# Kernel optimization log

Hardware: AMD Instinct MI355X
Metric: run time of the kernel (lower is better)

Reference implementation:

```python
import jax, jax.numpy as jnp
import numpy as np

B, S, D = 4, 512, 128


def setup_inputs() -> dict:
    key = jax.random.key(0)
    ks = jax.random.split(key, 9)
    scale = 1.0 / np.sqrt(D)
    return {
        "inputs": jax.random.normal(ks[0], (B, S, D), dtype=jnp.float32),
        "encoder_outputs": jax.random.normal(ks[1], (B, S, D), dtype=jnp.float32),
        "mask": jax.random.randint(ks[2], (B, S), 0, 2, dtype=jnp.int32),
        "W1": jax.random.uniform(ks[3], (D, D), jnp.float32, -scale, scale),
        "b1": jax.random.uniform(ks[4], (D,), jnp.float32, -scale, scale),
        "W2": jax.random.uniform(ks[5], (D, D), jnp.float32, -scale, scale),
        "b2": jax.random.uniform(ks[6], (D,), jnp.float32, -scale, scale),
        "v_w": jax.random.uniform(ks[7], (D,), jnp.float32, -scale, scale),
        "v_b": jax.random.uniform(ks[8], (1,), jnp.float32, -scale, scale),
    }


def reference(inputs, encoder_outputs, mask, W1, b1, W2, b2, v_w, v_b):
    # key_out: W1(encoder_outputs)  [B, S_k, D]
    key_out = jnp.einsum("bkd,de->bke", encoder_outputs, W1) + b1
    # query_out: W2(inputs)        [B, S_q, D]
    query_out = jnp.einsum("bqd,de->bqe", inputs, W2) + b2
    # additive attention, all query positions at once: [B, S_q, S_k, D]
    t = jnp.tanh(key_out[:, None, :, :] + query_out[:, :, None, :])
    ui = jnp.einsum("bqkd,d->bqk", t, v_w) + v_b[0]
    # mask out padded key positions for every query position
    valid = mask.astype(bool)[:, None, :]  # [B, 1, S_k]
    logits = jnp.where(valid, ui, -jnp.inf)
    preds = jnp.argmax(logits, axis=-1)
    return (logits, preds)
```

## Files before the change

### kernel.cpp

```cpp
#include <hip/hip_runtime.h>
#include <math.h>

#define NB 4
#define NS 512
#define ND 128
#define ND4 32

static constexpr float K2LE = 2.885390081777927f;

__device__ inline float fast_exp2(float x){
#if __has_builtin(__builtin_amdgcn_exp2f)
  return __builtin_amdgcn_exp2f(x);
#else
  float r; asm("v_exp_f32 %0, %1" : "=v"(r) : "v"(x)); return r;
#endif
}
__device__ inline float fast_rcp(float x){
#if __has_builtin(__builtin_amdgcn_rcpf)
  return __builtin_amdgcn_rcpf(x);
#else
  float r; asm("v_rcp_f32 %0, %1" : "=v"(r) : "v"(x)); return r;
#endif
}

__global__ __launch_bounds__(256) void proj_kernel(
    const float* __restrict__ inputs, const float* __restrict__ enc,
    const float* __restrict__ W1, const float* __restrict__ b1,
    const float* __restrict__ W2, const float* __restrict__ b2,
    const float* __restrict__ vw, const float* __restrict__ vb,
    float* __restrict__ EKT4, float* __restrict__ RQ, float* __restrict__ WQ,
    float* __restrict__ Csum){
  int blk = blockIdx.x;
  int t = threadIdx.x;

  if (blk == 512){
    if (t < 64){
      float v = vw[t] + vw[t + 64];
      #pragma unroll
      for (int off = 32; off; off >>= 1) v += __shfl_down(v, off);
      if (t == 0) Csum[0] = v + vb[0];
    }
    return;
  }

  bool is_key = (blk < 256);
  int rbase = (is_key ? blk : blk - 256) * 8;
  const float* X    = is_key ? enc : inputs;
  const float* W    = is_key ? W1  : W2;
  const float* bias = is_key ? b1  : b2;

  __shared__ float rows[8][132];
  {
    int r = t >> 5, c4 = (t & 31) * 4;
    *(float4*)&rows[r][c4] = *(const float4*)(X + (size_t)(rbase + r)*ND + c4);
  }
  __syncthreads();

  int rg = t >> 5;
  int ec = (t & 31) * 4;
  float4 acc = *(const float4*)(bias + ec);
  #pragma unroll 2
  for (int d4 = 0; d4 < ND4; ++d4){
    float4 x4 = *(const float4*)&rows[rg][4*d4];
    const float* wp = W + (size_t)(4*d4)*ND + ec;
    float4 w0 = *(const float4*)(wp);
    float4 w1 = *(const float4*)(wp + ND);
    float4 w2 = *(const float4*)(wp + 2*ND);
    float4 w3 = *(const float4*)(wp + 3*ND);
    acc.x = fmaf(x4.x, w0.x, acc.x); acc.y = fmaf(x4.x, w0.y, acc.y);
    acc.z = fmaf(x4.x, w0.z, acc.z); acc.w = fmaf(x4.x, w0.w, acc.w);
    acc.x = fmaf(x4.y, w1.x, acc.x); acc.y = fmaf(x4.y, w1.y, acc.y);
    acc.z = fmaf(x4.y, w1.z, acc.z); acc.w = fmaf(x4.y, w1.w, acc.w);
    acc.x = fmaf(x4.z, w2.x, acc.x); acc.y = fmaf(x4.z, w2.y, acc.y);
    acc.z = fmaf(x4.z, w2.z, acc.z); acc.w = fmaf(x4.z, w2.w, acc.w);
    acc.x = fmaf(x4.w, w3.x, acc.x); acc.y = fmaf(x4.w, w3.y, acc.y);
    acc.z = fmaf(x4.w, w3.z, acc.z); acc.w = fmaf(x4.w, w3.w, acc.w);
  }

  if (is_key){
    int b    = rbase >> 9;
    int sloc = rbase & (NS - 1);
    __syncthreads();
    rows[rg][ec+0] = fast_exp2(K2LE*acc.x);
    rows[rg][ec+1] = fast_exp2(K2LE*acc.y);
    rows[rg][ec+2] = fast_exp2(K2LE*acc.z);
    rows[rg][ec+3] = fast_exp2(K2LE*acc.w);
    __syncthreads();
    int d4 = t >> 3, sl = t & 7;
    float4 v = *(const float4*)&rows[sl][4*d4];
    ((float4*)EKT4)[((size_t)(b*ND4 + d4))*NS + sloc + sl] = v;
  } else {
    int row = rbase + rg;
    float4 vw4 = *(const float4*)(vw + ec);
    float4 r4, w4;
    r4.x = fast_exp2(-K2LE*acc.x);
    r4.y = fast_exp2(-K2LE*acc.y);
    r4.z = fast_exp2(-K2LE*acc.z);
    r4.w = fast_exp2(-K2LE*acc.w);
    w4.x = -2.0f*vw4.x*r4.x;
    w4.y = -2.0f*vw4.y*r4.y;
    w4.z = -2.0f*vw4.z*r4.z;
    w4.w = -2.0f*vw4.w*r4.w;
    *(float4*)(RQ + (size_t)row*ND + ec) = r4;
    *(float4*)(WQ + (size_t)row*ND + ec) = w4;
  }
}

__global__ __launch_bounds__(512) void score_kernel(
    const float* __restrict__ EKT4, const float* __restrict__ RQg,
    const float* __restrict__ WQg, const int* __restrict__ mask,
    const float* __restrict__ Csum, float* __restrict__ out){
  int blk = blockIdx.x;
  int b  = blk >> 7;
  int q0 = (blk & 127) * 4;
  int t  = threadIdx.x;

  const float4* ek4 = (const float4*)EKT4 + (size_t)(b*ND4)*NS + t;
  const float* rq = RQg + (size_t)(b*NS + q0)*ND;
  const float* wq = WQg + (size_t)(b*NS + q0)*ND;

  float C = Csum[0];
  int m = mask[b*NS + t];

  float a0=0.f, a1=0.f, a2=0.f, a3=0.f;
  #pragma unroll 2
  for (int d4 = 0; d4 < ND4; ++d4){
    float4 ek = ek4[(size_t)d4*NS];
    int d = 4*d4;
    float4 r0 = *(const float4*)(rq + d);
    float4 r1 = *(const float4*)(rq + ND + d);
    float4 r2 = *(const float4*)(rq + 2*ND + d);
    float4 r3 = *(const float4*)(rq + 3*ND + d);
    float4 w0 = *(const float4*)(wq + d);
    float4 w1 = *(const float4*)(wq + ND + d);
    float4 w2 = *(const float4*)(wq + 2*ND + d);
    float4 w3 = *(const float4*)(wq + 3*ND + d);
    a0 = fmaf(w0.x, fast_rcp(ek.x + r0.x), a0);
    a0 = fmaf(w0.y, fast_rcp(ek.y + r0.y), a0);
    a0 = fmaf(w0.z, fast_rcp(ek.z + r0.z), a0);
    a0 = fmaf(w0.w, fast_rcp(ek.w + r0.w), a0);
    a1 = fmaf(w1.x, fast_rcp(ek.x + r1.x), a1);
    a1 = fmaf(w1.y, fast_rcp(ek.y + r1.y), a1);
    a1 = fmaf(w1.z, fast_rcp(ek.z + r1.z), a1);
    a1 = fmaf(w1.w, fast_rcp(ek.w + r1.w), a1);
    a2 = fmaf(w2.x, fast_rcp(ek.x + r2.x), a2);
    a2 = fmaf(w2.y, fast_rcp(ek.y + r2.y), a2);
    a2 = fmaf(w2.z, fast_rcp(ek.z + r2.z), a2);
    a2 = fmaf(w2.w, fast_rcp(ek.w + r2.w), a2);
    a3 = fmaf(w3.x, fast_rcp(ek.x + r3.x), a3);
    a3 = fmaf(w3.y, fast_rcp(ek.y + r3.y), a3);
    a3 = fmaf(w3.z, fast_rcp(ek.z + r3.z), a3);
    a3 = fmaf(w3.w, fast_rcp(ek.w + r3.w), a3);
  }

  const float NINF = -3.0e38f;
  float u[4];
  u[0] = m ? (C + a0) : NINF;
  u[1] = m ? (C + a1) : NINF;
  u[2] = m ? (C + a2) : NINF;
  u[3] = m ? (C + a3) : NINF;

  float* logits = out;
  float* preds  = out + (size_t)NB*NS*NS;
  {
    size_t base = (size_t)(b*NS + q0) * NS + t;
    logits[base]        = u[0];
    logits[base +   NS] = u[1];
    logits[base + 2*NS] = u[2];
    logits[base + 3*NS] = u[3];
  }

  int lane = t & 63, wv = t >> 6;
  __shared__ float red_v[8][4];
  __shared__ int   red_i[8][4];
  #pragma unroll
  for (int qi = 0; qi < 4; ++qi){
    float v = u[qi]; int idx = t;
    #pragma unroll
    for (int off = 32; off; off >>= 1){
      float ov = __shfl_down(v, off);
      int   oi = __shfl_down(idx, off);
      if (ov > v || (ov == v && oi < idx)){ v = ov; idx = oi; }
    }
    if (lane == 0){ red_v[wv][qi] = v; red_i[wv][qi] = idx; }
  }
  __syncthreads();
  if (t < 4){
    float v = red_v[0][t]; int idx = red_i[0][t];
    #pragma unroll
    for (int w = 1; w < 8; ++w){
      float ov = red_v[w][t]; int oi = red_i[w][t];
      if (ov > v || (ov == v && oi < idx)){ v = ov; idx = oi; }
    }
    preds[b*NS + q0 + t] = (float)idx;
  }
}

extern "C" void kernel_launch(void* const* d_in, const int* in_sizes, int n_in,
                              void* d_out, int out_size, void* d_ws, size_t ws_size,
                              hipStream_t stream){
  const float* inputs = (const float*)d_in[0];
  const float* enc    = (const float*)d_in[1];
  const int*   mask   = (const int*)d_in[2];
  const float* W1     = (const float*)d_in[3];
  const float* b1     = (const float*)d_in[4];
  const float* W2     = (const float*)d_in[5];
  const float* b2     = (const float*)d_in[6];
  const float* vw     = (const float*)d_in[7];
  const float* vb     = (const float*)d_in[8];
  float* out = (float*)d_out;

  float* ws   = (float*)d_ws;
  float* EKT4 = ws;
  float* RQ   = ws + 262144;
  float* WQ   = ws + 524288;
  float* Cs   = ws + 786432;

  proj_kernel <<<dim3(513), dim3(256), 0, stream>>>(inputs, enc, W1, b1, W2, b2,
                                                    vw, vb, EKT4, RQ, WQ, Cs);
  score_kernel<<<dim3(512), dim3(512), 0, stream>>>(EKT4, RQ, WQ, mask, Cs, out);
}
```

Before: 99.72 us.

## Split score kernel over key tiles with atomic argmax merge

```diff
diff --git a/kernel.cpp b/kernel.cpp
--- a/kernel.cpp
+++ b/kernel.cpp
@@ -5,6 +5,8 @@
 #define NS 512
 #define ND 128
 #define ND4 32
+#define KT 256
+#define NKT (NS/KT)
 
 static constexpr float K2LE = 2.885390081777927f;
 
@@ -23,17 +25,24 @@
 #endif
 }
 
+__device__ inline unsigned enc_f32(float f){
+  unsigned u = __float_as_uint(f);
+  return (u & 0x80000000u) ? ~u : (u | 0x80000000u);
+}
+
 __global__ __launch_bounds__(256) void proj_kernel(
     const float* __restrict__ inputs, const float* __restrict__ enc,
     const float* __restrict__ W1, const float* __restrict__ b1,
     const float* __restrict__ W2, const float* __restrict__ b2,
     const float* __restrict__ vw, const float* __restrict__ vb,
     float* __restrict__ EKT4, float* __restrict__ RQ, float* __restrict__ WQ,
-    float* __restrict__ Csum){
+    float* __restrict__ Csum, unsigned long long* __restrict__ Amax){
   int blk = blockIdx.x;
   int t = threadIdx.x;
 
   if (blk == 512){
+    #pragma unroll
+    for (int i = t; i < NB*NS; i += 256) Amax[i] = 0ull;
     if (t < 64){
       float v = vw[t] + vw[t + 64];
       #pragma unroll
@@ -106,21 +115,25 @@
   }
 }
 
-__global__ __launch_bounds__(512) void score_kernel(
+__global__ __launch_bounds__(256) void score_kernel(
     const float* __restrict__ EKT4, const float* __restrict__ RQg,
     const float* __restrict__ WQg, const int* __restrict__ mask,
-    const float* __restrict__ Csum, float* __restrict__ out){
+    const float* __restrict__ Csum, float* __restrict__ out,
+    unsigned long long* __restrict__ Amax){
   int blk = blockIdx.x;
-  int b  = blk >> 7;
-  int q0 = (blk & 127) * 4;
-  int t  = threadIdx.x;
-
-  const float4* ek4 = (const float4*)EKT4 + (size_t)(b*ND4)*NS + t;
+  int b   = blk >> 8;
+  int rem = blk & 255;
+  int q0  = (rem >> 1) * 4;
+  int kt  = rem & 1;
+  int t   = threadIdx.x;
+  int k   = kt*KT + t;
+
+  const float4* ek4 = (const float4*)EKT4 + (size_t)(b*ND4)*NS + k;
   const float* rq = RQg + (size_t)(b*NS + q0)*ND;
   const float* wq = WQg + (size_t)(b*NS + q0)*ND;
 
   float C = Csum[0];
-  int m = mask[b*NS + t];
+  int m = mask[b*NS + k];
 
   float a0=0.f, a1=0.f, a2=0.f, a3=0.f;
   #pragma unroll 2
@@ -161,9 +174,8 @@
   u[3] = m ? (C + a3) : NINF;
 
   float* logits = out;
-  float* preds  = out + (size_t)NB*NS*NS;
   {
-    size_t base = (size_t)(b*NS + q0) * NS + t;
+    size_t base = (size_t)(b*NS + q0) * NS + k;
     logits[base]        = u[0];
     logits[base +   NS] = u[1];
     logits[base + 2*NS] = u[2];
@@ -171,11 +183,11 @@
   }
 
   int lane = t & 63, wv = t >> 6;
-  __shared__ float red_v[8][4];
-  __shared__ int   red_i[8][4];
+  __shared__ float red_v[4][4];
+  __shared__ int   red_i[4][4];
   #pragma unroll
   for (int qi = 0; qi < 4; ++qi){
-    float v = u[qi]; int idx = t;
+    float v = u[qi]; int idx = k;
     #pragma unroll
     for (int off = 32; off; off >>= 1){
       float ov = __shfl_down(v, off);
@@ -188,12 +200,23 @@
   if (t < 4){
     float v = red_v[0][t]; int idx = red_i[0][t];
     #pragma unroll
-    for (int w = 1; w < 8; ++w){
+    for (int w = 1; w < 4; ++w){
       float ov = red_v[w][t]; int oi = red_i[w][t];
       if (ov > v || (ov == v && oi < idx)){ v = ov; idx = oi; }
     }
-    preds[b*NS + q0 + t] = (float)idx;
-  }
+    unsigned long long key =
+        ((unsigned long long)enc_f32(v) << 32) |
+        (unsigned long long)(0xFFFFFFFFu - (unsigned)idx);
+    atomicMax(&Amax[b*NS + q0 + t], key);
+  }
+}
+
+__global__ __launch_bounds__(256) void finalize_kernel(
+    const unsigned long long* __restrict__ Amax, float* __restrict__ out){
+  int i = blockIdx.x * 256 + threadIdx.x;
+  float* preds = out + (size_t)NB*NS*NS;
+  unsigned idx = 0xFFFFFFFFu - (unsigned)(Amax[i] & 0xFFFFFFFFull);
+  preds[i] = (float)idx;
 }
 
 extern "C" void kernel_launch(void* const* d_in, const int* in_sizes, int n_in,
@@ -215,8 +238,10 @@
   float* RQ   = ws + 262144;
   float* WQ   = ws + 524288;
   float* Cs   = ws + 786432;
-
-  proj_kernel <<<dim3(513), dim3(256), 0, stream>>>(inputs, enc, W1, b1, W2, b2,
-                                                    vw, vb, EKT4, RQ, WQ, Cs);
-  score_kernel<<<dim3(512), dim3(512), 0, stream>>>(EKT4, RQ, WQ, mask, Cs, out);
-}
+  unsigned long long* Amax = (unsigned long long*)(ws + 786944);
+
+  proj_kernel    <<<dim3(513),  dim3(256), 0, stream>>>(inputs, enc, W1, b1, W2, b2,
+                                                        vw, vb, EKT4, RQ, WQ, Cs, Amax);
+  score_kernel   <<<dim3(1024), dim3(256), 0, stream>>>(EKT4, RQ, WQ, mask, Cs, out, Amax);
+  finalize_kernel<<<dim3(8),    dim3(256), 0, stream>>>(Amax, out);
+}
```

Result: slower. 111.6 us (+11.9%).
